# Kernel optimization log

Measured on AMD Instinct MI355X. Metric: run time of the kernel, lower is better.

Reference implementation:

```python
import jax, jax.numpy as jnp
import numpy as np
from jax import lax

B, T = 16384, 1000


def setup_inputs() -> dict:
    key = jax.random.key(0)
    k1, k2, k3, k4 = jax.random.split(key, 4)
    xicovs = jax.random.normal(k1, (B, T, 2, 2), dtype=jnp.float32) * 0.1
    dy = jax.random.normal(k2, (B, T, 2), dtype=jnp.float32) * 0.1
    coeffs_A = jax.random.normal(k3, (2, 2), dtype=jnp.float32) * 0.05
    C = jax.random.normal(k4, (2, 2), dtype=jnp.float32)
    x0 = jnp.zeros((B, 2), dtype=jnp.float32)
    dt = jnp.ones((1,), dtype=jnp.float32) * 0.001
    return {"xicovs": xicovs, "dy": dy, "coeffs_A": coeffs_A, "C": C, "x0": x0, "dt": dt}


def reference(xicovs, dy, coeffs_A, C, x0, dt):
    """Unrolls the GaussianDynamics recurrent cell over T steps with lax.scan.

    Per step (faithful to the original call):
      A_m  = coeffs_A - xicov @ C                     # [B,2,2]
      out  = (C @ x_prev) * dt                        # emitted output
      x    = x_prev + (A_m @ x_prev) * dt + xicov @ dy_t
    Returns (outputs [B,T,2], final_state [B,2]).
    """
    dts = dt[0]

    def step(x, inp):
        xic, dyt = inp  # [B,2,2], [B,2]
        A_m = coeffs_A - jnp.einsum('bij,jk->bik', xic, C)
        out = jnp.einsum('ij,bj->bi', C, x) * dts
        x_new = x + jnp.einsum('bij,bj->bi', A_m, x) * dts + jnp.einsum('bij,bj->bi', xic, dyt)
        return x_new, out

    xs = (jnp.moveaxis(xicovs, 1, 0), jnp.moveaxis(dy, 1, 0))  # time-major
    x_final, outs = lax.scan(step, x0, xs)
    return jnp.moveaxis(outs, 0, 1), x_final
```

## Files before the change

kernel.cpp:

```cpp
#include <hip/hip_runtime.h>


constexpr int BATCH = 16384;
constexpr int TLEN  = 1000;
constexpr int TPB   = 256;
constexpr int SPT   = 4;

typedef float vfloat4 __attribute__((ext_vector_type(4)));
typedef float vfloat2 __attribute__((ext_vector_type(2)));

template <int CTRL, int ROWMASK>
__device__ __forceinline__ float dppf(float oldv, float srcv) {
    return __int_as_float(__builtin_amdgcn_update_dpp(
        __float_as_int(oldv), __float_as_int(srcv), CTRL, ROWMASK, 0xf, false));
}

__global__ __launch_bounds__(TPB, 8) void gd_scan_kernel(
    const float* __restrict__ xicovs,
    const float* __restrict__ dyv,
    const float* __restrict__ cA,
    const float* __restrict__ Cm,
    const float* __restrict__ x0,
    const float* __restrict__ dtp,
    float* __restrict__ out)
{
    __shared__ vfloat4 s_xc[1024];
    __shared__ float wsum[TPB / 64][6];

    const int b    = blockIdx.x;
    const int tid  = threadIdx.x;
    const int lane = tid & 63;
    const int wv   = tid >> 6;

    const int t0  = tid * SPT;
    const int t0m = (t0 <= TLEN - SPT) ? t0 : (TLEN - SPT);
    const bool valid = (t0 < TLEN);

    const float* rowx = xicovs + (size_t)b * TLEN * 4;

#pragma unroll
    for (int k = 0; k < 4; ++k) {
        const int pw = k * 64 + lane;
        const int gw = pw ^ ((pw >> 3) & 7);
        int g = 256 * wv + gw;
        if (g > TLEN - 1) g = TLEN - 1;
        __builtin_amdgcn_global_load_lds(
            (const __attribute__((address_space(1))) void*)(rowx + (size_t)g * 4),
            (__attribute__((address_space(3))) void*)&s_xc[wv * 256 + k * 64],
            16, 0, 0);
    }

    const vfloat4* gd4 = reinterpret_cast<const vfloat4*>(dyv + (size_t)b * TLEN * 2);
    const vfloat4 dA = gd4[(t0m >> 1)];
    const vfloat4 dB = gd4[(t0m >> 1) + 1];

    const float dts = dtp[0];
    const vfloat2 CdColA = {Cm[0] * dts, Cm[2] * dts};
    const vfloat2 CdColB = {Cm[1] * dts, Cm[3] * dts};
    const vfloat2 nCdRow0 = {-Cm[0] * dts, -Cm[1] * dts};
    const vfloat2 nCdRow1 = {-Cm[2] * dts, -Cm[3] * dts};
    const vfloat2 AdRow0 = {1.f + cA[0] * dts, cA[1] * dts};
    const vfloat2 AdRow1 = {cA[2] * dts, 1.f + cA[3] * dts};
    const float xa = x0[2 * b], xb = x0[2 * b + 1];

    asm volatile("s_waitcnt vmcnt(0)" ::: "memory");

    vfloat4 xc[SPT];
#pragma unroll
    for (int s = 0; s < SPT; ++s) {
        const int gw  = 4 * lane + s;
        const int pos = gw ^ ((gw >> 3) & 7);
        xc[s] = s_xc[wv * 256 + pos];
    }
    const float dy0s[SPT] = {dA.x, dA.z, dB.x, dB.z};
    const float dy1s[SPT] = {dA.y, dA.w, dB.y, dB.w};

    vfloat2 Sa[SPT], Sb[SPT], ov[SPT];
    vfloat2 mA = {1.f, 0.f}, mB = {0.f, 1.f}, cc = {0.f, 0.f};
#pragma unroll
    for (int s = 0; s < SPT; ++s) {
        const vfloat4 xi = xc[s];
        const vfloat2 sa = AdRow0 + xi.x * nCdRow0 + xi.y * nCdRow1;
        const vfloat2 sb = AdRow1 + xi.z * nCdRow0 + xi.w * nCdRow1;
        const float o0 = xi.x * dy0s[s] + xi.y * dy1s[s];
        const float o1 = xi.z * dy0s[s] + xi.w * dy1s[s];
        Sa[s] = sa; Sb[s] = sb; ov[s] = vfloat2{o0, o1};
        const vfloat2 nA = sa.x * mA + sa.y * mB;
        const vfloat2 nB = sb.x * mA + sb.y * mB;
        const float nc0 = sa.x * cc.x + sa.y * cc.y + o0;
        const float nc1 = sb.x * cc.x + sb.y * cc.y + o1;
        mA = nA; mB = nB; cc = vfloat2{nc0, nc1};
    }
    if (!valid) { mA = vfloat2{1.f, 0.f}; mB = vfloat2{0.f, 1.f}; cc = vfloat2{0.f, 0.f}; }

#define SCAN_STEP(CTRL, RM)                                          \
    do {                                                             \
        vfloat2 smA, smB, scc;                                       \
        smA.x = dppf<CTRL, RM>(1.f, mA.x);                           \
        smA.y = dppf<CTRL, RM>(0.f, mA.y);                           \
        smB.x = dppf<CTRL, RM>(0.f, mB.x);                           \
        smB.y = dppf<CTRL, RM>(1.f, mB.y);                           \
        scc.x = dppf<CTRL, RM>(0.f, cc.x);                           \
        scc.y = dppf<CTRL, RM>(0.f, cc.y);                           \
        const vfloat2 nA = mA.x * smA + mA.y * smB;                  \
        const vfloat2 nB = mB.x * smA + mB.y * smB;                  \
        const float nc0 = mA.x * scc.x + mA.y * scc.y + cc.x;        \
        const float nc1 = mB.x * scc.x + mB.y * scc.y + cc.y;        \
        mA = nA; mB = nB; cc = vfloat2{nc0, nc1};                    \
    } while (0)

    SCAN_STEP(0x111, 0xf);
    SCAN_STEP(0x112, 0xf);
    SCAN_STEP(0x114, 0xf);
    SCAN_STEP(0x118, 0xf);
    SCAN_STEP(0x142, 0xa);
    SCAN_STEP(0x143, 0xc);
#undef SCAN_STEP

    if (lane == 63) {
        wsum[wv][0] = mA.x; wsum[wv][1] = mA.y;
        wsum[wv][2] = mB.x; wsum[wv][3] = mB.y;
        wsum[wv][4] = cc.x; wsum[wv][5] = cc.y;
    }
    __syncthreads();

    vfloat2 pA = {1.f, 0.f}, pB = {0.f, 1.f}, pc = {0.f, 0.f};
    for (int w = 0; w < wv; ++w) {
        const vfloat2 tA = {wsum[w][0], wsum[w][1]};
        const vfloat2 tB = {wsum[w][2], wsum[w][3]};
        const vfloat2 tc = {wsum[w][4], wsum[w][5]};
        const vfloat2 nA = tA.x * pA + tA.y * pB;
        const vfloat2 nB = tB.x * pA + tB.y * pB;
        const float nc0 = tA.x * pc.x + tA.y * pc.y + tc.x;
        const float nc1 = tB.x * pc.x + tB.y * pc.y + tc.y;
        pA = nA; pB = nB; pc = vfloat2{nc0, nc1};
    }

    vfloat2 eA, eB, ec;
    eA.x = __shfl_up(mA.x, 1); eA.y = __shfl_up(mA.y, 1);
    eB.x = __shfl_up(mB.x, 1); eB.y = __shfl_up(mB.y, 1);
    ec.x = __shfl_up(cc.x, 1); ec.y = __shfl_up(cc.y, 1);
    if (lane == 0) { eA = vfloat2{1.f, 0.f}; eB = vfloat2{0.f, 1.f}; ec = vfloat2{0.f, 0.f}; }

    const vfloat2 EA = eA.x * pA + eA.y * pB;
    const vfloat2 EB = eB.x * pA + eB.y * pB;
    const float Ec0 = eA.x * pc.x + eA.y * pc.y + ec.x;
    const float Ec1 = eB.x * pc.x + eB.y * pc.y + ec.y;

    float xq0 = EA.x * xa + EA.y * xb + Ec0;
    float xq1 = EB.x * xa + EB.y * xb + Ec1;

    vfloat2 op[SPT];
#pragma unroll
    for (int s = 0; s < SPT; ++s) {
        op[s] = xq0 * CdColA + xq1 * CdColB;
        const float nx0 = Sa[s].x * xq0 + Sa[s].y * xq1 + ov[s].x;
        const float nx1 = Sb[s].x * xq0 + Sb[s].y * xq1 + ov[s].y;
        xq0 = nx0; xq1 = nx1;
    }

    if (valid) {
        float* ob = out + (size_t)b * TLEN * 2 + (size_t)t0 * 2;
        vfloat4 w0 = {op[0].x, op[0].y, op[1].x, op[1].y};
        vfloat4 w1 = {op[2].x, op[2].y, op[3].x, op[3].y};
        __builtin_nontemporal_store(w0, reinterpret_cast<vfloat4*>(ob));
        __builtin_nontemporal_store(w1, reinterpret_cast<vfloat4*>(ob) + 1);
    }
    if (t0 == TLEN - SPT) {
        vfloat2 xf = {xq0, xq1};
        __builtin_nontemporal_store(
            xf, reinterpret_cast<vfloat2*>(out + (size_t)BATCH * TLEN * 2 + 2 * b));
    }
}

extern "C" void kernel_launch(void* const* d_in, const int* in_sizes, int n_in,
                              void* d_out, int out_size, void* d_ws, size_t ws_size,
                              hipStream_t stream) {
    const float* xicovs = (const float*)d_in[0];
    const float* dyv    = (const float*)d_in[1];
    const float* cA     = (const float*)d_in[2];
    const float* Cm     = (const float*)d_in[3];
    const float* x0     = (const float*)d_in[4];
    const float* dtp    = (const float*)d_in[5];
    float* out = (float*)d_out;

    gd_scan_kernel<<<BATCH, TPB, 0, stream>>>(xicovs, dyv, cA, Cm, x0, dtp, out);
}
```

Before: 97.60 us.

## Process eight batch rows per block with prefetch of the next row's inputs

Each block now handles eight consecutive batch rows instead of one, so the grid shrinks by a factor of eight. While one row is being computed, the next row's xicov tile is already streaming into LDS and its dy values into registers, with hand-placed waitcnt and sched_barrier calls ordering the work. A double-buffered wave-sum array means each row needs only one block barrier. The goal is to overlap global-load latency with compute and cut per-block launch overhead in a bandwidth-bound kernel. The cost is fewer blocks to spread across CUs and fragile manual vmcnt accounting that interleaved stores could disturb.

Result: slower. 195.0 us (+99.8%).

```diff
diff --git a/kernel.cpp b/kernel.cpp
--- a/kernel.cpp
+++ b/kernel.cpp
@@ -5,6 +5,8 @@
 constexpr int TLEN  = 1000;
 constexpr int TPB   = 256;
 constexpr int SPT   = 4;
+constexpr int ROWS  = 8;
+constexpr int NBLK  = BATCH / ROWS;
 
 typedef float vfloat4 __attribute__((ext_vector_type(4)));
 typedef float vfloat2 __attribute__((ext_vector_type(2)));
@@ -25,34 +27,39 @@
     float* __restrict__ out)
 {
     __shared__ vfloat4 s_xc[1024];
-    __shared__ float wsum[TPB / 64][6];
-
-    const int b    = blockIdx.x;
+    __shared__ float wsum[2][TPB / 64][6];
+
     const int tid  = threadIdx.x;
     const int lane = tid & 63;
     const int wv   = tid >> 6;
+    const int base = blockIdx.x * ROWS;
 
     const int t0  = tid * SPT;
     const int t0m = (t0 <= TLEN - SPT) ? t0 : (TLEN - SPT);
     const bool valid = (t0 < TLEN);
 
-    const float* rowx = xicovs + (size_t)b * TLEN * 4;
-
-#pragma unroll
-    for (int k = 0; k < 4; ++k) {
-        const int pw = k * 64 + lane;
-        const int gw = pw ^ ((pw >> 3) & 7);
-        int g = 256 * wv + gw;
-        if (g > TLEN - 1) g = TLEN - 1;
-        __builtin_amdgcn_global_load_lds(
-            (const __attribute__((address_space(1))) void*)(rowx + (size_t)g * 4),
-            (__attribute__((address_space(3))) void*)&s_xc[wv * 256 + k * 64],
-            16, 0, 0);
+#define STAGE_GL(RR)                                                            \
+    do {                                                                        \
+        const float* rowx_ = xicovs + (size_t)(RR) * (TLEN * 4);                \
+        _Pragma("unroll")                                                       \
+        for (int k = 0; k < 4; ++k) {                                           \
+            const int pw_ = k * 64 + lane;                                      \
+            const int gw_ = pw_ ^ ((pw_ >> 3) & 7);                             \
+            int g_ = 256 * wv + gw_;                                            \
+            if (g_ > TLEN - 1) g_ = TLEN - 1;                                   \
+            __builtin_amdgcn_global_load_lds(                                   \
+                (const __attribute__((address_space(1))) void*)(rowx_ + (size_t)g_ * 4), \
+                (__attribute__((address_space(3))) void*)&s_xc[wv * 256 + k * 64],       \
+                16, 0, 0);                                                      \
+        }                                                                       \
+    } while (0)
+
+    float x0s[2 * ROWS];
+#pragma unroll
+    for (int rr = 0; rr < ROWS; ++rr) {
+        x0s[2 * rr]     = x0[2 * (base + rr)];
+        x0s[2 * rr + 1] = x0[2 * (base + rr) + 1];
     }
-
-    const vfloat4* gd4 = reinterpret_cast<const vfloat4*>(dyv + (size_t)b * TLEN * 2);
-    const vfloat4 dA = gd4[(t0m >> 1)];
-    const vfloat4 dB = gd4[(t0m >> 1) + 1];
 
     const float dts = dtp[0];
     const vfloat2 CdColA = {Cm[0] * dts, Cm[2] * dts};
@@ -61,116 +68,146 @@
     const vfloat2 nCdRow1 = {-Cm[2] * dts, -Cm[3] * dts};
     const vfloat2 AdRow0 = {1.f + cA[0] * dts, cA[1] * dts};
     const vfloat2 AdRow1 = {cA[2] * dts, 1.f + cA[3] * dts};
-    const float xa = x0[2 * b], xb = x0[2 * b + 1];
-
-    asm volatile("s_waitcnt vmcnt(0)" ::: "memory");
-
-    vfloat4 xc[SPT];
-#pragma unroll
-    for (int s = 0; s < SPT; ++s) {
-        const int gw  = 4 * lane + s;
-        const int pos = gw ^ ((gw >> 3) & 7);
-        xc[s] = s_xc[wv * 256 + pos];
+
+    STAGE_GL(base);
+    __builtin_amdgcn_sched_barrier(0);
+    vfloat4 dyA = reinterpret_cast<const vfloat4*>(dyv + (size_t)base * (TLEN * 2))[t0m >> 1];
+    vfloat4 dyB = reinterpret_cast<const vfloat4*>(dyv + (size_t)base * (TLEN * 2))[(t0m >> 1) + 1];
+    __builtin_amdgcn_sched_barrier(0);
+
+#pragma unroll
+    for (int r = 0; r < ROWS; ++r) {
+        const int row = base + r;
+
+        if (r == 0) asm volatile("s_waitcnt vmcnt(2)" ::: "memory");
+        else        asm volatile("s_waitcnt vmcnt(4)" ::: "memory");
+        __builtin_amdgcn_sched_barrier(0);
+
+        vfloat4 xc[SPT];
+#pragma unroll
+        for (int s = 0; s < SPT; ++s) {
+            const int gw  = 4 * lane + s;
+            const int pos = gw ^ ((gw >> 3) & 7);
+            xc[s] = s_xc[wv * 256 + pos];
+        }
+        asm volatile("s_waitcnt lgkmcnt(0)" ::: "memory");
+        __builtin_amdgcn_sched_barrier(0);
+
+        vfloat4 dyAn = dyA, dyBn = dyB;
+        if (r + 1 < ROWS) {
+            STAGE_GL(row + 1);
+            const vfloat4* gdn = reinterpret_cast<const vfloat4*>(
+                dyv + (size_t)(row + 1) * (TLEN * 2));
+            dyAn = gdn[t0m >> 1];
+            dyBn = gdn[(t0m >> 1) + 1];
+        }
+        __builtin_amdgcn_sched_barrier(0);
+
+        const float dy0s[SPT] = {dyA.x, dyA.z, dyB.x, dyB.z};
+        const float dy1s[SPT] = {dyA.y, dyA.w, dyB.y, dyB.w};
+
+        vfloat2 Sa[SPT], Sb[SPT], ov[SPT];
+        vfloat2 mA = {1.f, 0.f}, mB = {0.f, 1.f}, cc = {0.f, 0.f};
+#pragma unroll
+        for (int s = 0; s < SPT; ++s) {
+            const vfloat4 xi = xc[s];
+            const vfloat2 sa = AdRow0 + xi.x * nCdRow0 + xi.y * nCdRow1;
+            const vfloat2 sb = AdRow1 + xi.z * nCdRow0 + xi.w * nCdRow1;
+            const float o0 = xi.x * dy0s[s] + xi.y * dy1s[s];
+            const float o1 = xi.z * dy0s[s] + xi.w * dy1s[s];
+            Sa[s] = sa; Sb[s] = sb; ov[s] = vfloat2{o0, o1};
+            const vfloat2 nA = sa.x * mA + sa.y * mB;
+            const vfloat2 nB = sb.x * mA + sb.y * mB;
+            const float nc0 = sa.x * cc.x + sa.y * cc.y + o0;
+            const float nc1 = sb.x * cc.x + sb.y * cc.y + o1;
+            mA = nA; mB = nB; cc = vfloat2{nc0, nc1};
+        }
+        if (!valid) { mA = vfloat2{1.f, 0.f}; mB = vfloat2{0.f, 1.f}; cc = vfloat2{0.f, 0.f}; }
+
+#define SCAN_STEP(CTRL, RM)                                          \
+        do {                                                         \
+            vfloat2 smA, smB, scc;                                   \
+            smA.x = dppf<CTRL, RM>(1.f, mA.x);                       \
+            smA.y = dppf<CTRL, RM>(0.f, mA.y);                       \
+            smB.x = dppf<CTRL, RM>(0.f, mB.x);                       \
+            smB.y = dppf<CTRL, RM>(1.f, mB.y);                       \
+            scc.x = dppf<CTRL, RM>(0.f, cc.x);                       \
+            scc.y = dppf<CTRL, RM>(0.f, cc.y);                       \
+            const vfloat2 nA = mA.x * smA + mA.y * smB;              \
+            const vfloat2 nB = mB.x * smA + mB.y * smB;              \
+            const float nc0 = mA.x * scc.x + mA.y * scc.y + cc.x;    \
+            const float nc1 = mB.x * scc.x + mB.y * scc.y + cc.y;    \
+            mA = nA; mB = nB; cc = vfloat2{nc0, nc1};                \
+        } while (0)
+
+        SCAN_STEP(0x111, 0xf);
+        SCAN_STEP(0x112, 0xf);
+        SCAN_STEP(0x114, 0xf);
+        SCAN_STEP(0x118, 0xf);
+        SCAN_STEP(0x142, 0xa);
+        SCAN_STEP(0x143, 0xc);
+#undef SCAN_STEP
+
+        const int pr = r & 1;
+        if (lane == 63) {
+            wsum[pr][wv][0] = mA.x; wsum[pr][wv][1] = mA.y;
+            wsum[pr][wv][2] = mB.x; wsum[pr][wv][3] = mB.y;
+            wsum[pr][wv][4] = cc.x; wsum[pr][wv][5] = cc.y;
+        }
+        asm volatile("s_waitcnt lgkmcnt(0)" ::: "memory");
+        __builtin_amdgcn_s_barrier();
+
+        vfloat2 pA = {1.f, 0.f}, pB = {0.f, 1.f}, pc = {0.f, 0.f};
+        for (int w = 0; w < wv; ++w) {
+            const vfloat2 tA = {wsum[pr][w][0], wsum[pr][w][1]};
+            const vfloat2 tB = {wsum[pr][w][2], wsum[pr][w][3]};
+            const vfloat2 tc = {wsum[pr][w][4], wsum[pr][w][5]};
+            const vfloat2 nA = tA.x * pA + tA.y * pB;
+            const vfloat2 nB = tB.x * pA + tB.y * pB;
+            const float nc0 = tA.x * pc.x + tA.y * pc.y + tc.x;
+            const float nc1 = tB.x * pc.x + tB.y * pc.y + tc.y;
+            pA = nA; pB = nB; pc = vfloat2{nc0, nc1};
+        }
+
+        vfloat2 eA, eB, ec;
+        eA.x = __shfl_up(mA.x, 1); eA.y = __shfl_up(mA.y, 1);
+        eB.x = __shfl_up(mB.x, 1); eB.y = __shfl_up(mB.y, 1);
+        ec.x = __shfl_up(cc.x, 1); ec.y = __shfl_up(cc.y, 1);
+        if (lane == 0) { eA = vfloat2{1.f, 0.f}; eB = vfloat2{0.f, 1.f}; ec = vfloat2{0.f, 0.f}; }
+
+        const vfloat2 EA = eA.x * pA + eA.y * pB;
+        const vfloat2 EB = eB.x * pA + eB.y * pB;
+        const float Ec0 = eA.x * pc.x + eA.y * pc.y + ec.x;
+        const float Ec1 = eB.x * pc.x + eB.y * pc.y + ec.y;
+
+        float xq0 = EA.x * x0s[2 * r] + EA.y * x0s[2 * r + 1] + Ec0;
+        float xq1 = EB.x * x0s[2 * r] + EB.y * x0s[2 * r + 1] + Ec1;
+
+        vfloat2 op[SPT];
+#pragma unroll
+        for (int s = 0; s < SPT; ++s) {
+            op[s] = xq0 * CdColA + xq1 * CdColB;
+            const float nx0 = Sa[s].x * xq0 + Sa[s].y * xq1 + ov[s].x;
+            const float nx1 = Sb[s].x * xq0 + Sb[s].y * xq1 + ov[s].y;
+            xq0 = nx0; xq1 = nx1;
+        }
+
+        if (valid) {
+            float* ob = out + (size_t)row * (TLEN * 2) + (size_t)t0 * 2;
+            vfloat4 w0 = {op[0].x, op[0].y, op[1].x, op[1].y};
+            vfloat4 w1 = {op[2].x, op[2].y, op[3].x, op[3].y};
+            __builtin_nontemporal_store(w0, reinterpret_cast<vfloat4*>(ob));
+            __builtin_nontemporal_store(w1, reinterpret_cast<vfloat4*>(ob) + 1);
+        }
+        if (t0 == TLEN - SPT) {
+            vfloat2 xf = {xq0, xq1};
+            __builtin_nontemporal_store(
+                xf, reinterpret_cast<vfloat2*>(out + (size_t)BATCH * (TLEN * 2) + 2 * row));
+        }
+
+        dyA = dyAn; dyB = dyBn;
     }
-    const float dy0s[SPT] = {dA.x, dA.z, dB.x, dB.z};
-    const float dy1s[SPT] = {dA.y, dA.w, dB.y, dB.w};
-
-    vfloat2 Sa[SPT], Sb[SPT], ov[SPT];
-    vfloat2 mA = {1.f, 0.f}, mB = {0.f, 1.f}, cc = {0.f, 0.f};
-#pragma unroll
-    for (int s = 0; s < SPT; ++s) {
-        const vfloat4 xi = xc[s];
-        const vfloat2 sa = AdRow0 + xi.x * nCdRow0 + xi.y * nCdRow1;
-        const vfloat2 sb = AdRow1 + xi.z * nCdRow0 + xi.w * nCdRow1;
-        const float o0 = xi.x * dy0s[s] + xi.y * dy1s[s];
-        const float o1 = xi.z * dy0s[s] + xi.w * dy1s[s];
-        Sa[s] = sa; Sb[s] = sb; ov[s] = vfloat2{o0, o1};
-        const vfloat2 nA = sa.x * mA + sa.y * mB;
-        const vfloat2 nB = sb.x * mA + sb.y * mB;
-        const float nc0 = sa.x * cc.x + sa.y * cc.y + o0;
-        const float nc1 = sb.x * cc.x + sb.y * cc.y + o1;
-        mA = nA; mB = nB; cc = vfloat2{nc0, nc1};
-    }
-    if (!valid) { mA = vfloat2{1.f, 0.f}; mB = vfloat2{0.f, 1.f}; cc = vfloat2{0.f, 0.f}; }
-
-#define SCAN_STEP(CTRL, RM)                                          \
-    do {                                                             \
-        vfloat2 smA, smB, scc;                                       \
-        smA.x = dppf<CTRL, RM>(1.f, mA.x);                           \
-        smA.y = dppf<CTRL, RM>(0.f, mA.y);                           \
-        smB.x = dppf<CTRL, RM>(0.f, mB.x);                           \
-        smB.y = dppf<CTRL, RM>(1.f, mB.y);                           \
-        scc.x = dppf<CTRL, RM>(0.f, cc.x);                           \
-        scc.y = dppf<CTRL, RM>(0.f, cc.y);                           \
-        const vfloat2 nA = mA.x * smA + mA.y * smB;                  \
-        const vfloat2 nB = mB.x * smA + mB.y * smB;                  \
-        const float nc0 = mA.x * scc.x + mA.y * scc.y + cc.x;        \
-        const float nc1 = mB.x * scc.x + mB.y * scc.y + cc.y;        \
-        mA = nA; mB = nB; cc = vfloat2{nc0, nc1};                    \
-    } while (0)
-
-    SCAN_STEP(0x111, 0xf);
-    SCAN_STEP(0x112, 0xf);
-    SCAN_STEP(0x114, 0xf);
-    SCAN_STEP(0x118, 0xf);
-    SCAN_STEP(0x142, 0xa);
-    SCAN_STEP(0x143, 0xc);
-#undef SCAN_STEP
-
-    if (lane == 63) {
-        wsum[wv][0] = mA.x; wsum[wv][1] = mA.y;
-        wsum[wv][2] = mB.x; wsum[wv][3] = mB.y;
-        wsum[wv][4] = cc.x; wsum[wv][5] = cc.y;
-    }
-    __syncthreads();
-
-    vfloat2 pA = {1.f, 0.f}, pB = {0.f, 1.f}, pc = {0.f, 0.f};
-    for (int w = 0; w < wv; ++w) {
-        const vfloat2 tA = {wsum[w][0], wsum[w][1]};
-        const vfloat2 tB = {wsum[w][2], wsum[w][3]};
-        const vfloat2 tc = {wsum[w][4], wsum[w][5]};
-        const vfloat2 nA = tA.x * pA + tA.y * pB;
-        const vfloat2 nB = tB.x * pA + tB.y * pB;
-        const float nc0 = tA.x * pc.x + tA.y * pc.y + tc.x;
-        const float nc1 = tB.x * pc.x + tB.y * pc.y + tc.y;
-        pA = nA; pB = nB; pc = vfloat2{nc0, nc1};
-    }
-
-    vfloat2 eA, eB, ec;
-    eA.x = __shfl_up(mA.x, 1); eA.y = __shfl_up(mA.y, 1);
-    eB.x = __shfl_up(mB.x, 1); eB.y = __shfl_up(mB.y, 1);
-    ec.x = __shfl_up(cc.x, 1); ec.y = __shfl_up(cc.y, 1);
-    if (lane == 0) { eA = vfloat2{1.f, 0.f}; eB = vfloat2{0.f, 1.f}; ec = vfloat2{0.f, 0.f}; }
-
-    const vfloat2 EA = eA.x * pA + eA.y * pB;
-    const vfloat2 EB = eB.x * pA + eB.y * pB;
-    const float Ec0 = eA.x * pc.x + eA.y * pc.y + ec.x;
-    const float Ec1 = eB.x * pc.x + eB.y * pc.y + ec.y;
-
-    float xq0 = EA.x * xa + EA.y * xb + Ec0;
-    float xq1 = EB.x * xa + EB.y * xb + Ec1;
-
-    vfloat2 op[SPT];
-#pragma unroll
-    for (int s = 0; s < SPT; ++s) {
-        op[s] = xq0 * CdColA + xq1 * CdColB;
-        const float nx0 = Sa[s].x * xq0 + Sa[s].y * xq1 + ov[s].x;
-        const float nx1 = Sb[s].x * xq0 + Sb[s].y * xq1 + ov[s].y;
-        xq0 = nx0; xq1 = nx1;
-    }
-
-    if (valid) {
-        float* ob = out + (size_t)b * TLEN * 2 + (size_t)t0 * 2;
-        vfloat4 w0 = {op[0].x, op[0].y, op[1].x, op[1].y};
-        vfloat4 w1 = {op[2].x, op[2].y, op[3].x, op[3].y};
-        __builtin_nontemporal_store(w0, reinterpret_cast<vfloat4*>(ob));
-        __builtin_nontemporal_store(w1, reinterpret_cast<vfloat4*>(ob) + 1);
-    }
-    if (t0 == TLEN - SPT) {
-        vfloat2 xf = {xq0, xq1};
-        __builtin_nontemporal_store(
-            xf, reinterpret_cast<vfloat2*>(out + (size_t)BATCH * TLEN * 2 + 2 * b));
-    }
+#undef STAGE_GL
 }
 
 extern "C" void kernel_launch(void* const* d_in, const int* in_sizes, int n_in,
@@ -184,5 +221,5 @@
     const float* dtp    = (const float*)d_in[5];
     float* out = (float*)d_out;
 
-    gd_scan_kernel<<<BATCH, TPB, 0, stream>>>(xicovs, dyv, cA, Cm, x0, dtp, out);
+    gd_scan_kernel<<<NBLK, TPB, 0, stream>>>(xicovs, dyv, cA, Cm, x0, dtp, out);
 }
```
